# Kernel tuning notes

Hardware: AMD Instinct MI355X
Metric: run time of the kernel (lower is better)

Reference implementation:

```python
import jax, jax.numpy as jnp
import numpy as np

N_NODES = 100000


def _gcn_layer(x, src, dst, deg_inv_sqrt, W, b):
    # GCNConv: out = D^{-1/2} (A + I) D^{-1/2} X W + b  (symmetric norm, self-loops)
    xw = x @ W  # [N, out]
    norm = deg_inv_sqrt[src] * deg_inv_sqrt[dst]  # [E]
    msg = xw[src] * norm[:, None]  # [E, out] gathered messages
    agg = jax.ops.segment_sum(msg, dst, num_segments=N_NODES)
    # self-loop contribution: norm_ii = deg_inv_sqrt[i]^2
    agg = agg + (deg_inv_sqrt * deg_inv_sqrt)[:, None] * xw
    return agg + b


def setup_inputs() -> dict:
    key = jax.random.key(0)
    k1, k2, k3, k4, k5, k6 = jax.random.split(key, 6)
    F_IN, HID, OUT, E = 128, 256, 40, 1600000
    x = jax.random.normal(k1, (N_NODES, F_IN), dtype=jnp.float32)
    edge_index = jax.random.randint(k2, (2, E), 0, N_NODES, dtype=jnp.int64)
    s1 = 1.0 / np.sqrt(F_IN)
    s2 = 1.0 / np.sqrt(HID)
    W1 = jax.random.uniform(k3, (F_IN, HID), jnp.float32, -s1, s1)
    b1 = jnp.zeros((HID,), jnp.float32)
    W2 = jax.random.uniform(k4, (HID, OUT), jnp.float32, -s2, s2)
    b2 = jnp.zeros((OUT,), jnp.float32)
    return {"x": x, "edge_index": edge_index, "W1": W1, "b1": b1, "W2": W2, "b2": b2}


def reference(x, edge_index, W1, b1, W2, b2):
    src, dst = edge_index[0], edge_index[1]
    # degree with self-loops (GCNConv default add_self_loops=True)
    deg = jax.ops.segment_sum(jnp.ones_like(dst, dtype=x.dtype), dst, num_segments=N_NODES) + 1.0
    deg_inv_sqrt = jax.lax.rsqrt(deg)
    h = _gcn_layer(x, src, dst, deg_inv_sqrt, W1, b1)
    h = jax.nn.relu(h)
    # dropout is identity in eval mode
    h = _gcn_layer(h, src, dst, deg_inv_sqrt, W2, b2)
    return jax.nn.log_softmax(h, axis=1)
```

## Files before the change

kernel.cpp:

```cpp
#include <hip/hip_runtime.h>
#include <math.h>

typedef long long ll;
typedef unsigned int uint;
typedef __attribute__((ext_vector_type(8))) short bf16x8;
typedef __attribute__((ext_vector_type(4))) float f32x4;

#define FIN 128
#define HID 256
#define FOUT 40
#define NG 8
#define NBIN 64
#define CAPPAD 65536

__device__ __forceinline__ float bflo(uint u) { return __uint_as_float(u << 16); }
__device__ __forceinline__ float bfhi(uint u) { return __uint_as_float(u & 0xFFFF0000u); }
__device__ __forceinline__ unsigned short f2bf(float f) {
  uint u = __float_as_uint(f);
  u += 0x7FFFu + ((u >> 16) & 1u);
  return (unsigned short)(u >> 16);
}

__device__ __forceinline__ int detect64(const uint* __restrict__ ei) {
  return (ei[1] == 0u && ei[3] == 0u && ei[5] == 0u && ei[7] == 0u) ? 1 : 0;
}

__global__ __launch_bounds__(256) void k_init(
    const void* __restrict__ ei,
    const float* __restrict__ W1, const float* __restrict__ W2,
    unsigned short* __restrict__ w1p, unsigned short* __restrict__ w2p,
    int2* __restrict__ partbuf, int* __restrict__ pcur,
    ll E, int range, ll cap) {
  __shared__ int lh[NG], lbase[NG];
  int t = threadIdx.x;
  int i = blockIdx.x * 256 + t;
  if (i < 32768) {
    int j = i & 7, g = (i >> 3) & 3, c = (i >> 5) & 255, s = i >> 13;
    int k = s * 32 + g * 8 + j;
    w1p[i] = f2bf(W1[(size_t)k * HID + c]);
  } else if (i < 32768 + 12288) {
    int i2 = i - 32768;
    int j = i2 & 7, g = (i2 >> 3) & 3, q = i2 >> 5;
    int c = q % 48, s = q / 48;
    int k = s * 32 + g * 8 + j;
    w2p[i2] = (c < FOUT) ? f2bf(W2[(size_t)k * FOUT + c]) : (unsigned short)0;
  }
  if (t < NG) lh[t] = 0;
  __syncthreads();

  int is64 = detect64((const uint*)ei);
  ll base = (ll)i * 4;
  int m = 0;
  int s[4], d[4], p[4], r[4];
  if (base < E) {
    m = (int)((E - base < 4) ? (E - base) : 4);
    if (is64) {
      if (m == 4) {
        longlong2 a0 = *(const longlong2*)((const ll*)ei + base);
        longlong2 a1 = *(const longlong2*)((const ll*)ei + base + 2);
        longlong2 b0 = *(const longlong2*)((const ll*)ei + E + base);
        longlong2 b1 = *(const longlong2*)((const ll*)ei + E + base + 2);
        s[0]=(int)a0.x; s[1]=(int)a0.y; s[2]=(int)a1.x; s[3]=(int)a1.y;
        d[0]=(int)b0.x; d[1]=(int)b0.y; d[2]=(int)b1.x; d[3]=(int)b1.y;
      } else {
        for (int j = 0; j < m; ++j) { s[j]=(int)((const ll*)ei)[base+j]; d[j]=(int)((const ll*)ei)[E+base+j]; }
      }
    } else {
      if (m == 4) {
        int4 a = *(const int4*)((const int*)ei + base);
        int4 b = *(const int4*)((const int*)ei + E + base);
        s[0]=a.x; s[1]=a.y; s[2]=a.z; s[3]=a.w;
        d[0]=b.x; d[1]=b.y; d[2]=b.z; d[3]=b.w;
      } else {
        for (int j = 0; j < m; ++j) { s[j]=((const int*)ei)[base+j]; d[j]=((const int*)ei)[E+base+j]; }
      }
    }
    for (int j = 0; j < m; ++j) {
      p[j] = d[j] / range;
      r[j] = atomicAdd(&lh[p[j]], 1);
    }
  }
  __syncthreads();
  if (t < NG) lbase[t] = lh[t] ? atomicAdd(&pcur[t], lh[t]) : 0;
  __syncthreads();
  for (int j = 0; j < m; ++j) {
    ll slot = (ll)lbase[p[j]] + r[j];
    if (slot < cap) partbuf[(ll)p[j] * cap + slot] = make_int2(s[j], d[j]);
  }
}

__global__ __launch_bounds__(256) void k_count(
    const int2* __restrict__ partbuf, const int* __restrict__ pcur,
    int* __restrict__ cnt, ll cap) {
  int g = blockIdx.x & (NG - 1);
  const int2* pb = partbuf + (ll)g * cap;
  int cnt_g = min(pcur[g], (int)cap);
  int bg = blockIdx.x >> 3, NB = gridDim.x >> 3;
  for (int i = bg * 256 + threadIdx.x; i < cnt_g; i += NB * 256) {
    int2 p = pb[i];
    atomicAdd(&cnt[p.y], 1);
  }
}

__global__ __launch_bounds__(1024) void k_scan1(const int* __restrict__ cnt,
                                                int* __restrict__ row_off,
                                                int* __restrict__ blksums, int n) {
  __shared__ int sm[1024];
  int t = threadIdx.x;
  int base = blockIdx.x * 4096 + t * 4;
  int v0 = (base + 0 < n) ? cnt[base + 0] : 0;
  int v1 = (base + 1 < n) ? cnt[base + 1] : 0;
  int v2 = (base + 2 < n) ? cnt[base + 2] : 0;
  int v3 = (base + 3 < n) ? cnt[base + 3] : 0;
  int s = v0 + v1 + v2 + v3;
  sm[t] = s;
  __syncthreads();
  for (int off = 1; off < 1024; off <<= 1) {
    int u = (t >= off) ? sm[t - off] : 0;
    __syncthreads();
    sm[t] += u;
    __syncthreads();
  }
  int excl = sm[t] - s;
  if (base + 0 < n) row_off[base + 0] = excl;
  if (base + 1 < n) row_off[base + 1] = excl + v0;
  if (base + 2 < n) row_off[base + 2] = excl + v0 + v1;
  if (base + 3 < n) row_off[base + 3] = excl + v0 + v1 + v2;
  if (t == 1023) blksums[blockIdx.x] = sm[1023];
}

__global__ void k_scan2(int* __restrict__ blksums, int nb) {
  if (threadIdx.x == 0 && blockIdx.x == 0) {
    int acc = 0;
    for (int i = 0; i < nb; ++i) { int v = blksums[i]; blksums[i] = acc; acc += v; }
    blksums[nb] = acc;
  }
}

__global__ __launch_bounds__(1024) void k_scan3(
    int* __restrict__ row_off, int* __restrict__ cursor,
    const int* __restrict__ blksums, float* __restrict__ dis,
    int* __restrict__ hist, int n, int nb) {
  __shared__ int lh[NBIN];
  int t = threadIdx.x;
  if (t < NBIN) lh[t] = 0;
  __syncthreads();
  int i = blockIdx.x * 1024 + t;
  if (i < n) {
    int c = cursor[i];
    int v = row_off[i] + blksums[i >> 12];
    row_off[i] = v;
    cursor[i] = v;
    dis[i] = rsqrtf((float)c + 1.0f);
    atomicAdd(&lh[min(c, NBIN - 1)], 1);
  }
  if (i == 0) row_off[n] = blksums[nb];
  __syncthreads();
  if (t < NBIN && lh[t]) atomicAdd(&hist[t], lh[t]);
}

__global__ void k_binpfx(const int* __restrict__ hist, int* __restrict__ bincur) {
  if (threadIdx.x == 0 && blockIdx.x == 0) {
    int acc = 0;
    for (int b = 0; b < NBIN; ++b) { int v = hist[b]; bincur[b] = acc; acc += v; }
  }
}

__global__ __launch_bounds__(256) void k_perm(
    const int* __restrict__ row_off, int* __restrict__ bincur,
    int* __restrict__ perm, int n) {
  __shared__ int lh[NBIN], lbase[NBIN];
  int t = threadIdx.x;
  if (t < NBIN) lh[t] = 0;
  __syncthreads();
  int base = blockIdx.x * 4096 + t * 16;
  int deg[16];
  #pragma unroll
  for (int j = 0; j < 16; ++j) {
    int i = base + j;
    if (i < n) {
      deg[j] = min(row_off[i + 1] - row_off[i], NBIN - 1);
      atomicAdd(&lh[deg[j]], 1);
    } else deg[j] = -1;
  }
  __syncthreads();
  if (t < NBIN) {
    lbase[t] = lh[t] ? atomicAdd(&bincur[t], lh[t]) : 0;
    lh[t] = 0;
  }
  __syncthreads();
  #pragma unroll
  for (int j = 0; j < 16; ++j) {
    if (deg[j] >= 0) {
      int r = atomicAdd(&lh[deg[j]], 1);
      perm[lbase[deg[j]] + r] = base + j;
    }
  }
}

__global__ __launch_bounds__(256) void k_fill(
    const int2* __restrict__ partbuf, const int* __restrict__ pcur,
    int* __restrict__ cursor, int* __restrict__ csr, ll cap) {
  int g = blockIdx.x & (NG - 1);
  const int2* pb = partbuf + (ll)g * cap;
  int cnt_g = min(pcur[g], (int)cap);
  int bg = blockIdx.x >> 3, NB = gridDim.x >> 3;
  for (int i = bg * 256 + threadIdx.x; i < cnt_g; i += NB * 256) {
    int2 p = pb[i];
    int pos = atomicAdd(&cursor[p.y], 1);
    csr[pos] = p.x;
  }
}

__global__ __launch_bounds__(256) void k_xcast(
    const float* __restrict__ x, const float* __restrict__ dis,
    unsigned short* __restrict__ xb, int total8) {
  int i = blockIdx.x * 256 + threadIdx.x;
  if (i >= total8) return;
  float w = dis[i >> 4];
  const float4* p = (const float4*)x + (size_t)i * 2;
  float4 a = p[0], b = p[1];
  uint4 o;
  o.x = (uint)f2bf(w * a.x) | ((uint)f2bf(w * a.y) << 16);
  o.y = (uint)f2bf(w * a.z) | ((uint)f2bf(w * a.w) << 16);
  o.z = (uint)f2bf(w * b.x) | ((uint)f2bf(w * b.y) << 16);
  o.w = (uint)f2bf(w * b.z) | ((uint)f2bf(w * b.w) << 16);
  *(uint4*)(xb + (size_t)i * 8) = o;
}

__device__ __forceinline__ void add8(float* a, uint4 r) {
  a[0] += bflo(r.x); a[1] += bfhi(r.x);
  a[2] += bflo(r.y); a[3] += bfhi(r.y);
  a[4] += bflo(r.z); a[5] += bfhi(r.z);
  a[6] += bflo(r.w); a[7] += bfhi(r.w);
}

__global__ __launch_bounds__(256) void k_fused1(
    const unsigned short* __restrict__ xb, const int* __restrict__ csr,
    const int* __restrict__ row_off, const float* __restrict__ dis,
    const int* __restrict__ perm,
    const unsigned short* __restrict__ w1p, const float* __restrict__ b1,
    const unsigned short* __restrict__ w2p, unsigned short* __restrict__ xw2b,
    int n)
{
  __shared__ __align__(16) unsigned short xsb[16 * 136];
  __shared__ __align__(16) unsigned short hsb[16 * 264];
  __shared__ int   nid[16];
  __shared__ float dsh[16];

  int tid = threadIdx.x;
  int n0 = (gridDim.x - 1 - blockIdx.x) * 16;
  int wv = tid >> 6, lane = tid & 63, qq = lane >> 4, l16 = lane & 15;
  int nl = wv * 4 + qq;
  int idx = n0 + nl;
  int node = (idx < n) ? perm[idx] : -1;

  float a[8] = {0, 0, 0, 0, 0, 0, 0, 0};
  float di = 0.f;
  if (node >= 0) {
    di = dis[node];
    uint4 v = *((const uint4*)(xb + (size_t)node * FIN) + l16);
    add8(a, v);
    int e0 = row_off[node], e1 = row_off[node + 1];
    int e = e0;
    for (; e + 8 <= e1; e += 8) {
      int s0 = csr[e],     s1 = csr[e + 1], s2 = csr[e + 2], s3 = csr[e + 3];
      int s4 = csr[e + 4], s5 = csr[e + 5], s6 = csr[e + 6], s7 = csr[e + 7];
      uint4 r0 = *((const uint4*)(xb + (size_t)s0 * FIN) + l16);
      uint4 r1 = *((const uint4*)(xb + (size_t)s1 * FIN) + l16);
      uint4 r2 = *((const uint4*)(xb + (size_t)s2 * FIN) + l16);
      uint4 r3 = *((const uint4*)(xb + (size_t)s3 * FIN) + l16);
      uint4 r4 = *((const uint4*)(xb + (size_t)s4 * FIN) + l16);
      uint4 r5 = *((const uint4*)(xb + (size_t)s5 * FIN) + l16);
      uint4 r6 = *((const uint4*)(xb + (size_t)s6 * FIN) + l16);
      uint4 r7 = *((const uint4*)(xb + (size_t)s7 * FIN) + l16);
      add8(a, r0); add8(a, r1); add8(a, r2); add8(a, r3);
      add8(a, r4); add8(a, r5); add8(a, r6); add8(a, r7);
    }
    for (; e < e1; ++e) {
      uint4 r0 = *((const uint4*)(xb + (size_t)csr[e] * FIN) + l16);
      add8(a, r0);
    }
  }
  if (l16 == 0) { nid[nl] = node; dsh[nl] = di; }
  {
    uint4 pk;
    pk.x = (uint)f2bf(di * a[0]) | ((uint)f2bf(di * a[1]) << 16);
    pk.y = (uint)f2bf(di * a[2]) | ((uint)f2bf(di * a[3]) << 16);
    pk.z = (uint)f2bf(di * a[4]) | ((uint)f2bf(di * a[5]) << 16);
    pk.w = (uint)f2bf(di * a[6]) | ((uint)f2bf(di * a[7]) << 16);
    *(uint4*)(xsb + nl * 136 + l16 * 8) = pk;
  }
  __syncthreads();

  int mrow = lane & 15, g = lane >> 4;
  f32x4 acc1[4] = {{0,0,0,0},{0,0,0,0},{0,0,0,0},{0,0,0,0}};
  #pragma unroll
  for (int s = 0; s < 4; ++s) {
    bf16x8 av = *(const bf16x8*)(xsb + mrow * 136 + s * 32 + g * 8);
    #pragma unroll
    for (int t = 0; t < 4; ++t) {
      int c = wv * 64 + t * 16 + mrow;
      bf16x8 bv = *(const bf16x8*)(w1p + (((size_t)(s * 256 + c) * 4 + g) << 3));
      acc1[t] = __builtin_amdgcn_mfma_f32_16x16x32_bf16(av, bv, acc1[t], 0, 0, 0);
    }
  }
  #pragma unroll
  for (int t = 0; t < 4; ++t) {
    int c = wv * 64 + t * 16 + mrow;
    float bb = b1[c];
    #pragma unroll
    for (int r = 0; r < 4; ++r) {
      float v = fmaxf(acc1[t][r] + bb, 0.f);
      hsb[(g * 4 + r) * 264 + c] = f2bf(v);
    }
  }
  __syncthreads();

  if (wv < 3) {
    f32x4 acc2 = {0, 0, 0, 0};
    int c2 = wv * 16 + mrow;
    #pragma unroll
    for (int s = 0; s < 8; ++s) {
      bf16x8 av = *(const bf16x8*)(hsb + mrow * 264 + s * 32 + g * 8);
      bf16x8 bv = *(const bf16x8*)(w2p + (((size_t)(s * 48 + c2) * 4 + g) << 3));
      acc2 = __builtin_amdgcn_mfma_f32_16x16x32_bf16(av, bv, acc2, 0, 0, 0);
    }
    if (c2 < FOUT) {
      #pragma unroll
      for (int r = 0; r < 4; ++r) {
        int nodeg = nid[g * 4 + r];
        if (nodeg >= 0)
          xw2b[(size_t)nodeg * FOUT + c2] = f2bf(acc2[r] * dsh[g * 4 + r]);
      }
    }
  }
}

__global__ __launch_bounds__(256) void k_layer2(
    const unsigned short* __restrict__ xw2b, const int* __restrict__ csr,
    const int* __restrict__ row_off, const float* __restrict__ dis,
    const int* __restrict__ perm,
    const float* __restrict__ b2, float* __restrict__ out, int n)
{
  int tid = threadIdx.x;
  int idx = (gridDim.x - 1 - blockIdx.x) * 16 + (tid >> 4);
  int l16 = tid & 15;
  if (idx >= n) return;
  int node = perm[idx];
  float di = dis[node];
  bool act = (l16 < 10);
  float a0 = 0.f, a1 = 0.f, a2 = 0.f, a3 = 0.f;
  if (act) {
    uint2 v = *((const uint2*)(xw2b + (size_t)node * FOUT) + l16);
    a0 = bflo(v.x); a1 = bfhi(v.x); a2 = bflo(v.y); a3 = bfhi(v.y);
  }
  int e0 = row_off[node], e1 = row_off[node + 1];
  int e = e0;
  for (; e + 8 <= e1; e += 8) {
    int s0 = csr[e],     s1 = csr[e + 1], s2 = csr[e + 2], s3 = csr[e + 3];
    int s4 = csr[e + 4], s5 = csr[e + 5], s6 = csr[e + 6], s7 = csr[e + 7];
    if (act) {
      uint2 r0 = *((const uint2*)(xw2b + (size_t)s0 * FOUT) + l16);
      uint2 r1 = *((const uint2*)(xw2b + (size_t)s1 * FOUT) + l16);
      uint2 r2 = *((const uint2*)(xw2b + (size_t)s2 * FOUT) + l16);
      uint2 r3 = *((const uint2*)(xw2b + (size_t)s3 * FOUT) + l16);
      uint2 r4 = *((const uint2*)(xw2b + (size_t)s4 * FOUT) + l16);
      uint2 r5 = *((const uint2*)(xw2b + (size_t)s5 * FOUT) + l16);
      uint2 r6 = *((const uint2*)(xw2b + (size_t)s6 * FOUT) + l16);
      uint2 r7 = *((const uint2*)(xw2b + (size_t)s7 * FOUT) + l16);
      a0 += bflo(r0.x); a1 += bfhi(r0.x); a2 += bflo(r0.y); a3 += bfhi(r0.y);
      a0 += bflo(r1.x); a1 += bfhi(r1.x); a2 += bflo(r1.y); a3 += bfhi(r1.y);
      a0 += bflo(r2.x); a1 += bfhi(r2.x); a2 += bflo(r2.y); a3 += bfhi(r2.y);
      a0 += bflo(r3.x); a1 += bfhi(r3.x); a2 += bflo(r3.y); a3 += bfhi(r3.y);
      a0 += bflo(r4.x); a1 += bfhi(r4.x); a2 += bflo(r4.y); a3 += bfhi(r4.y);
      a0 += bflo(r5.x); a1 += bfhi(r5.x); a2 += bflo(r5.y); a3 += bfhi(r5.y);
      a0 += bflo(r6.x); a1 += bfhi(r6.x); a2 += bflo(r6.y); a3 += bfhi(r6.y);
      a0 += bflo(r7.x); a1 += bfhi(r7.x); a2 += bflo(r7.y); a3 += bfhi(r7.y);
    }
  }
  for (; e < e1; ++e) {
    int s0 = csr[e];
    if (act) {
      uint2 r0 = *((const uint2*)(xw2b + (size_t)s0 * FOUT) + l16);
      a0 += bflo(r0.x); a1 += bfhi(r0.x); a2 += bflo(r0.y); a3 += bfhi(r0.y);
    }
  }
  float l0 = -INFINITY, l1 = -INFINITY, l2 = -INFINITY, l3 = -INFINITY;
  if (act) {
    float4 bv = *(const float4*)(b2 + l16 * 4);
    l0 = di * a0 + bv.x; l1 = di * a1 + bv.y;
    l2 = di * a2 + bv.z; l3 = di * a3 + bv.w;
  }
  float m = fmaxf(fmaxf(l0, l1), fmaxf(l2, l3));
  #pragma unroll
  for (int off = 8; off > 0; off >>= 1) m = fmaxf(m, __shfl_xor(m, off));
  float s = 0.f;
  if (act) s = expf(l0 - m) + expf(l1 - m) + expf(l2 - m) + expf(l3 - m);
  #pragma unroll
  for (int off = 8; off > 0; off >>= 1) s += __shfl_xor(s, off);
  if (act) {
    float ls = m + logf(s);
    float4 o = make_float4(l0 - ls, l1 - ls, l2 - ls, l3 - ls);
    *(float4*)(out + (size_t)node * FOUT + l16 * 4) = o;
  }
}

extern "C" void kernel_launch(void* const* d_in, const int* in_sizes, int n_in,
                              void* d_out, int out_size, void* d_ws, size_t ws_size,
                              hipStream_t stream) {
  const float* x  = (const float*)d_in[0];
  const void*  ei = d_in[1];
  const float* W1 = (const float*)d_in[2];
  const float* b1 = (const float*)d_in[3];
  const float* W2 = (const float*)d_in[4];
  const float* b2 = (const float*)d_in[5];
  float* out = (float*)d_out;

  int n = in_sizes[0] / FIN;
  ll  E = (ll)in_sizes[1] / 2;
  int nb = (n + 4095) / 4096;
  int range = (n + NG - 1) / NG;
  ll  cap = E / NG + CAPPAD;

  char* ws = (char*)d_ws;
  size_t off = 0;
  auto carve = [&](size_t bytes) -> char* {
    char* p = ws + off;
    off = (off + bytes + 255) & ~(size_t)255;
    return p;
  };
  int*   row_off = (int*)carve((size_t)(n + 1) * 4);
  int*   cursor  = (int*)carve((size_t)n * 4);
  int2*  partbuf = (int2*)carve((size_t)NG * cap * 8);
  int*   pcur    = (int*)carve(NG * 4);
  int*   csr     = (int*)carve((size_t)E * 4);
  int*   blksums = (int*)carve(64 * 4);
  int*   hist    = (int*)carve(NBIN * 4);
  int*   bincur  = (int*)carve(NBIN * 4);
  int*   perm    = (int*)carve((size_t)n * 4);
  float* dis     = (float*)carve((size_t)n * 4);
  unsigned short* xb   = (unsigned short*)carve((size_t)n * FIN * 2);
  unsigned short* w1p  = (unsigned short*)carve(32768 * 2);
  unsigned short* w2p  = (unsigned short*)carve(12288 * 2);
  unsigned short* xw2b = (unsigned short*)carve((size_t)n * FOUT * 2);
  (void)n_in; (void)out_size; (void)ws_size;

  int gx8   = (n * FIN / 8 + 255) / 256;
  int gt16  = (n + 15) / 16;
  int gperm = (n + 4095) / 4096;
  int ginit = (int)((E + 1023) / 1024);

  hipMemsetAsync(cursor, 0, (size_t)n * 4, stream);
  hipMemsetAsync(hist, 0, NBIN * 4, stream);
  hipMemsetAsync(pcur, 0, NG * 4, stream);

  hipLaunchKernelGGL(k_init,  dim3(ginit), dim3(256), 0, stream,
                     ei, W1, W2, w1p, w2p, partbuf, pcur, E, range, cap);
  hipLaunchKernelGGL(k_count, dim3(2048), dim3(256), 0, stream, partbuf, pcur, cursor, cap);
  hipLaunchKernelGGL(k_scan1, dim3(nb), dim3(1024), 0, stream, cursor, row_off, blksums, n);
  hipLaunchKernelGGL(k_scan2, dim3(1), dim3(1), 0, stream, blksums, nb);
  hipLaunchKernelGGL(k_scan3, dim3((n + 1023) / 1024), dim3(1024), 0, stream,
                     row_off, cursor, blksums, dis, hist, n, nb);
  hipLaunchKernelGGL(k_binpfx, dim3(1), dim3(1), 0, stream, hist, bincur);
  hipLaunchKernelGGL(k_perm,  dim3(gperm), dim3(256), 0, stream, row_off, bincur, perm, n);
  hipLaunchKernelGGL(k_fill,  dim3(2048), dim3(256), 0, stream, partbuf, pcur, cursor, csr, cap);
  hipLaunchKernelGGL(k_xcast, dim3(gx8), dim3(256), 0, stream, x, dis, xb, n * FIN / 8);
  hipLaunchKernelGGL(k_fused1, dim3(gt16), dim3(256), 0, stream,
                     xb, csr, row_off, dis, perm, w1p, b1, w2p, xw2b, n);
  hipLaunchKernelGGL(k_layer2, dim3(gt16), dim3(256), 0, stream,
                     xw2b, csr, row_off, dis, perm, b2, out, n);
}
```

Measured before the change: 328.3 us.

## Use wave ballot ranking in partition, fold bin prefix into perm, merge memsets

The edge partition kernel now ranks edges per group with wave ballots and popcounts, plus per-wave prefix sums, in place of shared-memory atomics. The single-thread bin-prefix kernel is removed and each k_perm block recomputes the prefix from the histogram itself. The three memsets become one over a contiguous zeroed region. The layer kernels now walk nodes in forward perm order instead of reversed, which changes the order in which high- and low-degree nodes are scheduled and may affect load balance.

Result: faster. 312.9 us (-4.7%).

```diff
diff --git a/kernel.cpp b/kernel.cpp
--- a/kernel.cpp
+++ b/kernel.cpp
@@ -31,9 +31,11 @@
     unsigned short* __restrict__ w1p, unsigned short* __restrict__ w2p,
     int2* __restrict__ partbuf, int* __restrict__ pcur,
     ll E, int range, ll cap) {
-  __shared__ int lh[NG], lbase[NG];
+  __shared__ int wrun[4][NG], wbase[4][NG], lbase[NG];
   int t = threadIdx.x;
   int i = blockIdx.x * 256 + t;
+  int lane = t & 63, w = t >> 6;
+
   if (i < 32768) {
     int j = i & 7, g = (i >> 3) & 3, c = (i >> 5) & 255, s = i >> 13;
     int k = s * 32 + g * 8 + j;
@@ -45,13 +47,11 @@
     int k = s * 32 + g * 8 + j;
     w2p[i2] = (c < FOUT) ? f2bf(W2[(size_t)k * FOUT + c]) : (unsigned short)0;
   }
-  if (t < NG) lh[t] = 0;
-  __syncthreads();
 
   int is64 = detect64((const uint*)ei);
   ll base = (ll)i * 4;
   int m = 0;
-  int s[4], d[4], p[4], r[4];
+  int s[4], d[4], p[4] = {-1, -1, -1, -1};
   if (base < E) {
     m = (int)((E - base < 4) ? (E - base) : 4);
     if (is64) {
@@ -75,17 +75,33 @@
         for (int j = 0; j < m; ++j) { s[j]=((const int*)ei)[base+j]; d[j]=((const int*)ei)[E+base+j]; }
       }
     }
-    for (int j = 0; j < m; ++j) {
-      p[j] = d[j] / range;
-      r[j] = atomicAdd(&lh[p[j]], 1);
-    }
-  }
-  __syncthreads();
-  if (t < NG) lbase[t] = lh[t] ? atomicAdd(&pcur[t], lh[t]) : 0;
+    for (int j = 0; j < m; ++j) p[j] = d[j] / range;
+  }
+
+  int run[NG] = {0,0,0,0,0,0,0,0};
+  int rank[4] = {0,0,0,0};
+  unsigned long long lt = (1ull << lane) - 1ull;
+  #pragma unroll
+  for (int j = 0; j < 4; ++j) {
+    #pragma unroll
+    for (int g = 0; g < NG; ++g) {
+      unsigned long long mm = __ballot(p[j] == g);
+      if (p[j] == g) rank[j] = run[g] + (int)__popcll(mm & lt);
+      run[g] += (int)__popcll(mm);
+    }
+  }
+  if (lane < NG) wrun[w][lane] = run[lane];
+  __syncthreads();
+  if (t < NG) {
+    int acc = 0;
+    for (int ww = 0; ww < 4; ++ww) { wbase[ww][t] = acc; acc += wrun[ww][t]; }
+    lbase[t] = acc ? atomicAdd(&pcur[t], acc) : 0;
+  }
   __syncthreads();
   for (int j = 0; j < m; ++j) {
-    ll slot = (ll)lbase[p[j]] + r[j];
-    if (slot < cap) partbuf[(ll)p[j] * cap + slot] = make_int2(s[j], d[j]);
+    int g = p[j];
+    ll slot = (ll)lbase[g] + wbase[w][g] + rank[j];
+    if (slot < cap) partbuf[(ll)g * cap + slot] = make_int2(s[j], d[j]);
   }
 }
 
@@ -159,20 +175,17 @@
   if (t < NBIN && lh[t]) atomicAdd(&hist[t], lh[t]);
 }
 
-__global__ void k_binpfx(const int* __restrict__ hist, int* __restrict__ bincur) {
-  if (threadIdx.x == 0 && blockIdx.x == 0) {
+__global__ __launch_bounds__(256) void k_perm(
+    const int* __restrict__ row_off, const int* __restrict__ hist,
+    int* __restrict__ pbincur, int* __restrict__ perm, int n) {
+  __shared__ int lh[NBIN], lbase[NBIN], pfx[NBIN];
+  int t = threadIdx.x;
+  if (t < NBIN) { lh[t] = 0; pfx[t] = hist[t]; }
+  __syncthreads();
+  if (t == 0) {
     int acc = 0;
-    for (int b = 0; b < NBIN; ++b) { int v = hist[b]; bincur[b] = acc; acc += v; }
-  }
-}
-
-__global__ __launch_bounds__(256) void k_perm(
-    const int* __restrict__ row_off, int* __restrict__ bincur,
-    int* __restrict__ perm, int n) {
-  __shared__ int lh[NBIN], lbase[NBIN];
-  int t = threadIdx.x;
-  if (t < NBIN) lh[t] = 0;
-  __syncthreads();
+    for (int b = 0; b < NBIN; ++b) { int v = pfx[b]; pfx[b] = acc; acc += v; }
+  }
   int base = blockIdx.x * 4096 + t * 16;
   int deg[16];
   #pragma unroll
@@ -185,7 +198,7 @@
   }
   __syncthreads();
   if (t < NBIN) {
-    lbase[t] = lh[t] ? atomicAdd(&bincur[t], lh[t]) : 0;
+    lbase[t] = pfx[t] + (lh[t] ? atomicAdd(&pbincur[t], lh[t]) : 0);
     lh[t] = 0;
   }
   __syncthreads();
@@ -249,7 +262,7 @@
   __shared__ float dsh[16];
 
   int tid = threadIdx.x;
-  int n0 = (gridDim.x - 1 - blockIdx.x) * 16;
+  int n0 = blockIdx.x * 16;
   int wv = tid >> 6, lane = tid & 63, qq = lane >> 4, l16 = lane & 15;
   int nl = wv * 4 + qq;
   int idx = n0 + nl;
@@ -344,7 +357,7 @@
     const float* __restrict__ b2, float* __restrict__ out, int n)
 {
   int tid = threadIdx.x;
-  int idx = (gridDim.x - 1 - blockIdx.x) * 16 + (tid >> 4);
+  int idx = blockIdx.x * 16 + (tid >> 4);
   int l16 = tid & 15;
   if (idx >= n) return;
   int node = perm[idx];
@@ -430,14 +443,16 @@
     off = (off + bytes + 255) & ~(size_t)255;
     return p;
   };
+  int zn = n + NBIN + NBIN + NG;
+  int*   zbase   = (int*)carve((size_t)zn * 4);
+  int*   cursor  = zbase;
+  int*   hist    = zbase + n;
+  int*   pbincur = zbase + n + NBIN;
+  int*   pcur    = zbase + n + NBIN + NBIN;
   int*   row_off = (int*)carve((size_t)(n + 1) * 4);
-  int*   cursor  = (int*)carve((size_t)n * 4);
   int2*  partbuf = (int2*)carve((size_t)NG * cap * 8);
-  int*   pcur    = (int*)carve(NG * 4);
   int*   csr     = (int*)carve((size_t)E * 4);
   int*   blksums = (int*)carve(64 * 4);
-  int*   hist    = (int*)carve(NBIN * 4);
-  int*   bincur  = (int*)carve(NBIN * 4);
   int*   perm    = (int*)carve((size_t)n * 4);
   float* dis     = (float*)carve((size_t)n * 4);
   unsigned short* xb   = (unsigned short*)carve((size_t)n * FIN * 2);
@@ -451,9 +466,7 @@
   int gperm = (n + 4095) / 4096;
   int ginit = (int)((E + 1023) / 1024);
 
-  hipMemsetAsync(cursor, 0, (size_t)n * 4, stream);
-  hipMemsetAsync(hist, 0, NBIN * 4, stream);
-  hipMemsetAsync(pcur, 0, NG * 4, stream);
+  hipMemsetAsync(zbase, 0, (size_t)zn * 4, stream);
 
   hipLaunchKernelGGL(k_init,  dim3(ginit), dim3(256), 0, stream,
                      ei, W1, W2, w1p, w2p, partbuf, pcur, E, range, cap);
@@ -462,8 +475,8 @@
   hipLaunchKernelGGL(k_scan2, dim3(1), dim3(1), 0, stream, blksums, nb);
   hipLaunchKernelGGL(k_scan3, dim3((n + 1023) / 1024), dim3(1024), 0, stream,
                      row_off, cursor, blksums, dis, hist, n, nb);
-  hipLaunchKernelGGL(k_binpfx, dim3(1), dim3(1), 0, stream, hist, bincur);
-  hipLaunchKernelGGL(k_perm,  dim3(gperm), dim3(256), 0, stream, row_off, bincur, perm, n);
+  hipLaunchKernelGGL(k_perm,  dim3(gperm), dim3(256), 0, stream,
+                     row_off, hist, pbincur, perm, n);
   hipLaunchKernelGGL(k_fill,  dim3(2048), dim3(256), 0, stream, partbuf, pcur, cursor, csr, cap);
   hipLaunchKernelGGL(k_xcast, dim3(gx8), dim3(256), 0, stream, x, dis, xb, n * FIN / 8);
   hipLaunchKernelGGL(k_fused1, dim3(gt16), dim3(256), 0, stream,
```
